# Kernel optimization log

Measured on AMD Instinct MI355X. Metric: run time of the kernel, lower is better.

The kernel has to match this reference:

```python
import jax, jax.numpy as jnp
import numpy as np

EMBED = 1024
HEADS = 16
DIM_HEAD = EMBED // HEADS
N, L = 4, 2048


def setup_inputs() -> dict:
    key = jax.random.key(0)
    ks = jax.random.split(key, 12)
    s = 0.02
    return {
        "q": jax.random.normal(ks[0], (N, L, EMBED), jnp.float32),
        "k": jax.random.normal(ks[1], (N, L, EMBED), jnp.float32),
        "v": jax.random.normal(ks[2], (N, L, EMBED), jnp.float32),
        "padding_mask": jnp.ones((N, L), dtype=bool),
        "sequence_mask": jnp.zeros((L, L), dtype=bool),
        # Linear(in, out): store weight as [out, in] like torch, bias [out]
        "Wq": jax.random.normal(ks[3], (EMBED, EMBED), jnp.float32) * s,
        "bq": jnp.zeros((EMBED,), jnp.float32),
        "Wk": jax.random.normal(ks[4], (EMBED, EMBED), jnp.float32) * s,
        "bk": jnp.zeros((EMBED,), jnp.float32),
        "Wv": jax.random.normal(ks[5], (EMBED, EMBED), jnp.float32) * s,
        "bv": jnp.zeros((EMBED,), jnp.float32),
        "Wo": jax.random.normal(ks[6], (EMBED, EMBED), jnp.float32) * s,
        "bo": jnp.zeros((EMBED,), jnp.float32),
    }


def reference(q, k, v, padding_mask, sequence_mask, Wq, bq, Wk, bk, Wv, bv, Wo, bo):
    n, lq, _ = q.shape
    lk = k.shape[1]
    # input projections
    qp = (q @ Wq.T + bq).reshape(n, lq, HEADS, DIM_HEAD)
    kp = (k @ Wk.T + bk).reshape(n, lk, HEADS, DIM_HEAD)
    vp = (v @ Wv.T + bv).reshape(n, lk, HEADS, DIM_HEAD)
    # energy: [n, h, lq, lk]
    energy = jnp.einsum('nqhd,nkhd->nhqk', qp, kp)
    attention = jax.nn.softmax(energy / jnp.sqrt(jnp.float32(EMBED)), axis=3)
    # NOTE: the original torch code calls masked_fill (non in-place) and
    # discards the result, so padding_mask / sequence_mask have NO effect.
    # Dropout is also never applied in forward. Replicated faithfully.
    out = jnp.einsum('nhqk,nkhd->nqhd', attention, vp)
    out = out.reshape(n, lq, EMBED)
    return out @ Wo.T + bo
```

## Files before the change

kernel.cpp:

```cpp
#include <hip/hip_runtime.h>
#include <stdint.h>

typedef _Float16 f16;
typedef _Float16 f16x8 __attribute__((ext_vector_type(8)));
typedef _Float16 f16x4 __attribute__((ext_vector_type(4)));
typedef _Float16 f16x2 __attribute__((ext_vector_type(2)));
typedef float f32x4 __attribute__((ext_vector_type(4)));

__device__ __forceinline__ f32x4 mfma16(f16x8 a, f16x8 b, f32x4 c) {
    return __builtin_amdgcn_mfma_f32_16x16x32_f16(a, b, c, 0, 0, 0);
}

__device__ __forceinline__ void gload16(const f16* g, f16* l) {
    __builtin_amdgcn_global_load_lds(
        (const __attribute__((address_space(1))) uint32_t*)g,
        (__attribute__((address_space(3))) uint32_t*)l, 16, 0, 0);
}

template <bool OUT16>
__device__ __forceinline__ void gemm_body(const f16* __restrict__ A,
                                          const f16* __restrict__ B,
                                          const float* __restrict__ bias,
                                          void* __restrict__ Cout, long ldo,
                                          int biasrow, float scale,
                                          long m0, long n0, f16* As, f16* Bs) {
    int tid = threadIdx.x;
    int lane = tid & 63, w = tid >> 6;
    int wm = w & 1, wn = w >> 1;
    int l15 = lane & 15, quad = lane >> 4;

    int rg = lane >> 3;
    int cg = (lane & 7) ^ rg;
    const f16* ag[4];
    const f16* bg[4];
    f16* al[4];
    f16* bl[4];
#pragma unroll
    for (int t = 0; t < 4; ++t) {
        int rb = (w * 4 + t) * 8;
        ag[t] = A + (m0 + rb + rg) * 1024 + cg * 8;
        bg[t] = B + (n0 + rb + rg) * 1024 + cg * 8;
        al[t] = &As[rb * 64];
        bl[t] = &Bs[rb * 64];
    }

    f32x4 acc[4][4] = {};

    for (int k0 = 0; k0 < 1024; k0 += 64) {
        __syncthreads();
#pragma unroll
        for (int t = 0; t < 4; ++t) {
            gload16(ag[t] + k0, al[t]);
            gload16(bg[t] + k0, bl[t]);
        }
        __syncthreads();
#pragma unroll
        for (int ks = 0; ks < 2; ++ks) {
            int cc = (ks * 4 + quad) ^ (l15 & 7);
            f16x8 af[4], bf[4];
#pragma unroll
            for (int t = 0; t < 4; ++t) {
                af[t] = *(const f16x8*)&As[(wm * 64 + t * 16 + l15) * 64 + cc * 8];
                bf[t] = *(const f16x8*)&Bs[(wn * 64 + t * 16 + l15) * 64 + cc * 8];
            }
#pragma unroll
            for (int i = 0; i < 4; ++i)
#pragma unroll
                for (int j = 0; j < 4; ++j)
                    acc[i][j] = mfma16(af[i], bf[j], acc[i][j]);
        }
    }

#pragma unroll
    for (int i = 0; i < 4; ++i) {
        int mrow = wm * 64 + i * 16 + quad * 4;
#pragma unroll
        for (int j = 0; j < 4; ++j) {
            int ncol = wn * 64 + j * 16 + l15;
            long gn = n0 + ncol;
#pragma unroll
            for (int r = 0; r < 4; ++r) {
                long gm = m0 + mrow + r;
                float v = (acc[i][j][r] + (biasrow ? bias[gm] : bias[gn])) * scale;
                if constexpr (OUT16)
                    ((f16*)Cout)[gm * ldo + gn] = (f16)v;
                else
                    ((float*)Cout)[gm * ldo + gn] = v;
            }
        }
    }
}

__global__ __launch_bounds__(256, 2) void qkv_proj(
    const f16* __restrict__ qh, const f16* __restrict__ kh,
    const f16* __restrict__ vh, const f16* __restrict__ Wh,
    const float* __restrict__ bq, const float* __restrict__ bk,
    const float* __restrict__ bv, f16* __restrict__ Qp, f16* __restrict__ Kp,
    f16* __restrict__ Vt) {
    __shared__ __align__(16) f16 As[128 * 64];
    __shared__ __align__(16) f16 Bs[128 * 64];
    int z = blockIdx.z;
    const f16* A;
    const f16* B;
    const float* bias;
    f16* C;
    long ldo;
    int biasrow;
    float scale;
    if (z == 0) {
        A = qh; B = Wh; bias = bq; C = Qp; ldo = 1024; biasrow = 0;
        scale = 0.0450842200277786f;
    } else if (z == 1) {
        A = kh; B = Wh + 1048576; bias = bk; C = Kp; ldo = 1024; biasrow = 0;
        scale = 1.0f;
    } else {
        A = Wh + 2097152; B = vh; bias = bv; C = Vt; ldo = 8192; biasrow = 1;
        scale = 1.0f;
    }
    long m0 = (long)(z == 2 ? blockIdx.y : blockIdx.x) * 128;
    long n0 = (long)(z == 2 ? blockIdx.x : blockIdx.y) * 128;
    gemm_body<true>(A, B, bias, C, ldo, biasrow, scale, m0, n0, As, Bs);
}

__global__ __launch_bounds__(256, 2) void o_proj(const f16* __restrict__ Op,
                                                 const f16* __restrict__ Wo,
                                                 const float* __restrict__ bo,
                                                 float* __restrict__ out) {
    __shared__ __align__(16) f16 As[128 * 64];
    __shared__ __align__(16) f16 Bs[128 * 64];
    gemm_body<false>(Op, Wo, bo, out, 1024, 0, 1.0f, (long)blockIdx.x * 128,
                     (long)blockIdx.y * 128, As, Bs);
}

__global__ __launch_bounds__(256, 2) void attn256(const f16* __restrict__ Qp,
                                                  const f16* __restrict__ Kp,
                                                  const f16* __restrict__ Vt,
                                                  f16* __restrict__ Op) {
    __shared__ __align__(16) f16 Ps0[128 * 64];
    __shared__ __align__(16) f16 Ps1[128 * 64];
    __shared__ __align__(16) f16 Ks[2][64 * 64];
    __shared__ __align__(16) f16 Vs[2][64 * 64];

    int tid = threadIdx.x;
    int lane = tid & 63, w = tid >> 6;
    int l15 = lane & 15, quad = lane >> 4;
    int b = blockIdx.x;
    int xcd = b & 7, slot = b >> 3;
    int nh = xcd * 8 + (slot >> 3);
    int qp = slot & 7;
    int nb = nh >> 4, h = nh & 15;
    long tok0 = (long)nb * 2048;
    long qrow0 = qp * 256;

    int rg = lane >> 3, cg = (lane & 7) ^ rg;

    const f16* qsrc0 = Qp + (tok0 + qrow0) * 1024 + h * 64;
    const f16* qsrc1 = qsrc0 + 128 * 1024;
#pragma unroll
    for (int t = 0; t < 4; ++t) {
        int rb = w * 32 + t * 8;
        gload16(qsrc0 + (rb + rg) * 1024 + cg * 8, &Ps0[rb * 64]);
        gload16(qsrc1 + (rb + rg) * 1024 + cg * 8, &Ps1[rb * 64]);
    }
    const f16* kptr = Kp + (tok0 + w * 16 + rg) * 1024 + h * 64 + cg * 8;
    const f16* vptr = Vt + ((long)h * 64 + w * 16 + rg) * 8192 + tok0 + cg * 8;
    gload16(kptr, &Ks[0][(w * 16) * 64]);
    gload16(kptr + 8 * 1024, &Ks[0][(w * 16 + 8) * 64]);
    gload16(vptr, &Vs[0][(w * 16) * 64]);
    gload16(vptr + (long)8 * 8192, &Vs[0][(w * 16 + 8) * 64]);
    const f16* kn = kptr + 65536;
    const f16* vn = vptr + 64;
    __syncthreads();

    f16x8 qf0[2][2], qf1[2][2];
#pragma unroll
    for (int ks = 0; ks < 2; ++ks) {
        int cc = (ks * 4 + quad) ^ (l15 & 7);
#pragma unroll
        for (int j = 0; j < 2; ++j) {
            qf0[ks][j] = *(const f16x8*)&Ps0[(w * 32 + j * 16 + l15) * 64 + cc * 8];
            qf1[ks][j] = *(const f16x8*)&Ps1[(w * 32 + j * 16 + l15) * 64 + cc * 8];
        }
    }

    f32x4 oacc0[2][4] = {}, oacc1[2][4] = {};
    float rs0[2] = {0.f, 0.f}, rs1[2] = {0.f, 0.f};
    const f32x4 z4 = {0.f, 0.f, 0.f, 0.f};

    for (int kt = 0; kt < 32; ++kt) {
        int cur = kt & 1;
        f32x4 sacc0[4][2], sacc1[4][2];
#pragma unroll
        for (int ks = 0; ks < 2; ++ks) {
            int cc = (ks * 4 + quad) ^ (l15 & 7);
            f16x8 a[4];
#pragma unroll
            for (int t = 0; t < 4; ++t)
                a[t] = *(const f16x8*)&Ks[cur][(t * 16 + l15) * 64 + cc * 8];
#pragma unroll
            for (int i = 0; i < 4; ++i)
#pragma unroll
                for (int j = 0; j < 2; ++j) {
                    if (ks == 0) {
                        sacc0[i][j] = mfma16(a[i], qf0[0][j], z4);
                        sacc1[i][j] = mfma16(a[i], qf1[0][j], z4);
                    } else {
                        sacc0[i][j] = mfma16(a[i], qf0[1][j], sacc0[i][j]);
                        sacc1[i][j] = mfma16(a[i], qf1[1][j], sacc1[i][j]);
                    }
                }
        }
        if (kt < 31) {
            int nxt = cur ^ 1;
            f16* kd = &Ks[nxt][(w * 16) * 64];
            f16* vd = &Vs[nxt][(w * 16) * 64];
            gload16(kn, kd);
            gload16(kn + 8 * 1024, kd + 8 * 64);
            gload16(vn, vd);
            gload16(vn + (long)8 * 8192, vd + 8 * 64);
            kn += 65536;
            vn += 64;
        }
#pragma unroll
        for (int i = 0; i < 4; ++i) {
#pragma unroll
            for (int j = 0; j < 2; ++j) {
                int qrow = w * 32 + j * 16 + l15;
                int kl = i * 16 + quad * 4;
                int c = kl >> 3;
                int off = qrow * 64 + ((c ^ (qrow & 7)) << 3) + (kl & 7);
                {
                    float p0 = __builtin_amdgcn_exp2f(sacc0[i][j][0]);
                    float p1 = __builtin_amdgcn_exp2f(sacc0[i][j][1]);
                    float p2 = __builtin_amdgcn_exp2f(sacc0[i][j][2]);
                    float p3 = __builtin_amdgcn_exp2f(sacc0[i][j][3]);
                    rs0[j] += (p0 + p1) + (p2 + p3);
                    f16x2 lo = __builtin_bit_cast(f16x2, __builtin_amdgcn_cvt_pkrtz(p0, p1));
                    f16x2 hi = __builtin_bit_cast(f16x2, __builtin_amdgcn_cvt_pkrtz(p2, p3));
                    f16x4 ph;
                    ph[0] = lo[0]; ph[1] = lo[1]; ph[2] = hi[0]; ph[3] = hi[1];
                    *(f16x4*)&Ps0[off] = ph;
                }
                {
                    float p0 = __builtin_amdgcn_exp2f(sacc1[i][j][0]);
                    float p1 = __builtin_amdgcn_exp2f(sacc1[i][j][1]);
                    float p2 = __builtin_amdgcn_exp2f(sacc1[i][j][2]);
                    float p3 = __builtin_amdgcn_exp2f(sacc1[i][j][3]);
                    rs1[j] += (p0 + p1) + (p2 + p3);
                    f16x2 lo = __builtin_bit_cast(f16x2, __builtin_amdgcn_cvt_pkrtz(p0, p1));
                    f16x2 hi = __builtin_bit_cast(f16x2, __builtin_amdgcn_cvt_pkrtz(p2, p3));
                    f16x4 ph;
                    ph[0] = lo[0]; ph[1] = lo[1]; ph[2] = hi[0]; ph[3] = hi[1];
                    *(f16x4*)&Ps1[off] = ph;
                }
            }
        }
#pragma unroll
        for (int ks = 0; ks < 2; ++ks) {
            int cc = (ks * 4 + quad) ^ (l15 & 7);
            f16x8 bf[4];
#pragma unroll
            for (int j = 0; j < 4; ++j)
                bf[j] = *(const f16x8*)&Vs[cur][(j * 16 + l15) * 64 + cc * 8];
            f16x8 af0[2], af1[2];
#pragma unroll
            for (int i = 0; i < 2; ++i) {
                af0[i] = *(const f16x8*)&Ps0[(w * 32 + i * 16 + l15) * 64 + cc * 8];
                af1[i] = *(const f16x8*)&Ps1[(w * 32 + i * 16 + l15) * 64 + cc * 8];
            }
#pragma unroll
            for (int i = 0; i < 2; ++i)
#pragma unroll
                for (int j = 0; j < 4; ++j) {
                    oacc0[i][j] = mfma16(af0[i], bf[j], oacc0[i][j]);
                    oacc1[i][j] = mfma16(af1[i], bf[j], oacc1[i][j]);
                }
        }
        __syncthreads();
    }

    float* lsi = (float*)&Ks[0][0];
#pragma unroll
    for (int j = 0; j < 2; ++j) {
        rs0[j] += __shfl_xor(rs0[j], 16, 64);
        rs0[j] += __shfl_xor(rs0[j], 32, 64);
        rs1[j] += __shfl_xor(rs1[j], 16, 64);
        rs1[j] += __shfl_xor(rs1[j], 32, 64);
    }
    if (lane < 16) {
        lsi[w * 32 + lane] = 1.0f / rs0[0];
        lsi[w * 32 + 16 + lane] = 1.0f / rs0[1];
        lsi[128 + w * 32 + lane] = 1.0f / rs1[0];
        lsi[128 + w * 32 + 16 + lane] = 1.0f / rs1[1];
    }

    long otok = tok0 + qrow0;
#pragma unroll
    for (int i = 0; i < 2; ++i) {
        int qrow = w * 32 + i * 16 + quad * 4;
#pragma unroll
        for (int j = 0; j < 4; ++j) {
            int d = j * 16 + l15;
#pragma unroll
            for (int r = 0; r < 4; ++r) {
                Op[(otok + qrow + r) * 1024 + h * 64 + d] =
                    (f16)(oacc0[i][j][r] * lsi[qrow + r]);
                Op[(otok + 128 + qrow + r) * 1024 + h * 64 + d] =
                    (f16)(oacc1[i][j][r] * lsi[128 + qrow + r]);
            }
        }
    }
}

__global__ void cvt_all(const float* __restrict__ q, const float* __restrict__ k,
                        const float* __restrict__ v, const float* __restrict__ w0,
                        const float* __restrict__ w1, const float* __restrict__ w2,
                        const float* __restrict__ w3, f16* __restrict__ qh,
                        f16* __restrict__ kh, f16* __restrict__ vh,
                        f16* __restrict__ wh) {
    long id = (long)blockIdx.x * 256 + threadIdx.x;
    const float* s;
    f16* d;
    long off;
    if (id < 3145728) {
        int which = (int)(id >> 20);
        off = (id & 1048575) * 8;
        s = which == 0 ? q : which == 1 ? k : v;
        d = which == 0 ? qh : which == 1 ? kh : vh;
    } else {
        long id2 = id - 3145728;
        int wi = (int)(id2 >> 17);
        off = (id2 & 131071) * 8;
        s = wi == 0 ? w0 : wi == 1 ? w1 : wi == 2 ? w2 : w3;
        d = wh + (long)wi * 1048576;
    }
    f32x4 a = *(const f32x4*)(s + off);
    f32x4 b = *(const f32x4*)(s + off + 4);
    f16x8 hv;
    hv[0] = (f16)a[0]; hv[1] = (f16)a[1]; hv[2] = (f16)a[2]; hv[3] = (f16)a[3];
    hv[4] = (f16)b[0]; hv[5] = (f16)b[1]; hv[6] = (f16)b[2]; hv[7] = (f16)b[3];
    *(f16x8*)(d + off) = hv;
}

extern "C" void kernel_launch(void* const* d_in, const int* in_sizes, int n_in,
                              void* d_out, int out_size, void* d_ws, size_t ws_size,
                              hipStream_t stream) {
    const float* q  = (const float*)d_in[0];
    const float* k  = (const float*)d_in[1];
    const float* v  = (const float*)d_in[2];
    const float* Wq = (const float*)d_in[5];
    const float* bq = (const float*)d_in[6];
    const float* Wk = (const float*)d_in[7];
    const float* bk = (const float*)d_in[8];
    const float* Wv = (const float*)d_in[9];
    const float* bv = (const float*)d_in[10];
    const float* Wo = (const float*)d_in[11];
    const float* bo = (const float*)d_in[12];

    char* ws = (char*)d_ws;
    f16* qh = (f16*)ws;
    f16* kh = (f16*)(ws + (16L << 20));
    f16* vh = (f16*)(ws + (32L << 20));
    f16* Wh = (f16*)(ws + (48L << 20));
    f16* Qp = (f16*)(ws + (56L << 20));
    f16* Kp = (f16*)(ws + (72L << 20));
    f16* Vt = (f16*)(ws + (88L << 20));
    f16* Op = (f16*)(ws + (104L << 20));

    cvt_all<<<14336, 256, 0, stream>>>(q, k, v, Wq, Wk, Wv, Wo, qh, kh, vh, Wh);

    qkv_proj<<<dim3(64, 8, 3), 256, 0, stream>>>(qh, kh, vh, Wh, bq, bk, bv,
                                                 Qp, Kp, Vt);

    attn256<<<512, 256, 0, stream>>>(Qp, Kp, Vt, Op);

    o_proj<<<dim3(64, 8), 256, 0, stream>>>(Op, Wh + 3145728, bo, (float*)d_out);
}
```

Before: 340.2 us.

## Share one P buffer across two query halves to fit three attention blocks per CU

Attention now uses a single P tile in LDS instead of two. The second query half is staged through the unused K/V double-buffer slots at startup, and its exp/PV phase is serialized after the first half's. This cuts LDS per block so launch bounds can request three blocks per CU instead of two. It also adds s_setprio around the MFMA sections to favour matrix work across waves. The cost is more serialization inside each iteration and higher register pressure under the tighter occupancy bound.

```diff
diff --git a/kernel.cpp b/kernel.cpp
--- a/kernel.cpp
+++ b/kernel.cpp
@@ -132,12 +132,11 @@
                      (long)blockIdx.y * 128, As, Bs);
 }
 
-__global__ __launch_bounds__(256, 2) void attn256(const f16* __restrict__ Qp,
+__global__ __launch_bounds__(256, 3) void attn256(const f16* __restrict__ Qp,
                                                   const f16* __restrict__ Kp,
                                                   const f16* __restrict__ Vt,
                                                   f16* __restrict__ Op) {
-    __shared__ __align__(16) f16 Ps0[128 * 64];
-    __shared__ __align__(16) f16 Ps1[128 * 64];
+    __shared__ __align__(16) f16 Ps[128 * 64];
     __shared__ __align__(16) f16 Ks[2][64 * 64];
     __shared__ __align__(16) f16 Vs[2][64 * 64];
 
@@ -159,8 +158,9 @@
 #pragma unroll
     for (int t = 0; t < 4; ++t) {
         int rb = w * 32 + t * 8;
-        gload16(qsrc0 + (rb + rg) * 1024 + cg * 8, &Ps0[rb * 64]);
-        gload16(qsrc1 + (rb + rg) * 1024 + cg * 8, &Ps1[rb * 64]);
+        gload16(qsrc0 + (rb + rg) * 1024 + cg * 8, &Ps[rb * 64]);
+        f16* q1d = (rb < 64) ? &Ks[1][rb * 64] : &Vs[1][(rb - 64) * 64];
+        gload16(qsrc1 + (rb + rg) * 1024 + cg * 8, q1d);
     }
     const f16* kptr = Kp + (tok0 + w * 16 + rg) * 1024 + h * 64 + cg * 8;
     const f16* vptr = Vt + ((long)h * 64 + w * 16 + rg) * 8192 + tok0 + cg * 8;
@@ -173,15 +173,19 @@
     __syncthreads();
 
     f16x8 qf0[2][2], qf1[2][2];
+    const f16* q1b = (w < 2) ? &Ks[1][0] : &Vs[1][0];
+    int q1off = (w < 2) ? 0 : 64;
 #pragma unroll
     for (int ks = 0; ks < 2; ++ks) {
         int cc = (ks * 4 + quad) ^ (l15 & 7);
 #pragma unroll
         for (int j = 0; j < 2; ++j) {
-            qf0[ks][j] = *(const f16x8*)&Ps0[(w * 32 + j * 16 + l15) * 64 + cc * 8];
-            qf1[ks][j] = *(const f16x8*)&Ps1[(w * 32 + j * 16 + l15) * 64 + cc * 8];
-        }
-    }
+            int row = w * 32 + j * 16 + l15;
+            qf0[ks][j] = *(const f16x8*)&Ps[row * 64 + cc * 8];
+            qf1[ks][j] = *(const f16x8*)&q1b[(row - q1off) * 64 + cc * 8];
+        }
+    }
+    __syncthreads();
 
     f32x4 oacc0[2][4] = {}, oacc1[2][4] = {};
     float rs0[2] = {0.f, 0.f}, rs1[2] = {0.f, 0.f};
@@ -190,6 +194,7 @@
     for (int kt = 0; kt < 32; ++kt) {
         int cur = kt & 1;
         f32x4 sacc0[4][2], sacc1[4][2];
+        __builtin_amdgcn_s_setprio(1);
 #pragma unroll
         for (int ks = 0; ks < 2; ++ks) {
             int cc = (ks * 4 + quad) ^ (l15 & 7);
@@ -210,6 +215,7 @@
                     }
                 }
         }
+        __builtin_amdgcn_s_setprio(0);
         if (kt < 31) {
             int nxt = cur ^ 1;
             f16* kd = &Ks[nxt][(w * 16) * 64];
@@ -229,32 +235,19 @@
                 int kl = i * 16 + quad * 4;
                 int c = kl >> 3;
                 int off = qrow * 64 + ((c ^ (qrow & 7)) << 3) + (kl & 7);
-                {
-                    float p0 = __builtin_amdgcn_exp2f(sacc0[i][j][0]);
-                    float p1 = __builtin_amdgcn_exp2f(sacc0[i][j][1]);
-                    float p2 = __builtin_amdgcn_exp2f(sacc0[i][j][2]);
-                    float p3 = __builtin_amdgcn_exp2f(sacc0[i][j][3]);
-                    rs0[j] += (p0 + p1) + (p2 + p3);
-                    f16x2 lo = __builtin_bit_cast(f16x2, __builtin_amdgcn_cvt_pkrtz(p0, p1));
-                    f16x2 hi = __builtin_bit_cast(f16x2, __builtin_amdgcn_cvt_pkrtz(p2, p3));
-                    f16x4 ph;
-                    ph[0] = lo[0]; ph[1] = lo[1]; ph[2] = hi[0]; ph[3] = hi[1];
-                    *(f16x4*)&Ps0[off] = ph;
-                }
-                {
-                    float p0 = __builtin_amdgcn_exp2f(sacc1[i][j][0]);
-                    float p1 = __builtin_amdgcn_exp2f(sacc1[i][j][1]);
-                    float p2 = __builtin_amdgcn_exp2f(sacc1[i][j][2]);
-                    float p3 = __builtin_amdgcn_exp2f(sacc1[i][j][3]);
-                    rs1[j] += (p0 + p1) + (p2 + p3);
-                    f16x2 lo = __builtin_bit_cast(f16x2, __builtin_amdgcn_cvt_pkrtz(p0, p1));
-                    f16x2 hi = __builtin_bit_cast(f16x2, __builtin_amdgcn_cvt_pkrtz(p2, p3));
-                    f16x4 ph;
-                    ph[0] = lo[0]; ph[1] = lo[1]; ph[2] = hi[0]; ph[3] = hi[1];
-                    *(f16x4*)&Ps1[off] = ph;
-                }
+                float p0 = __builtin_amdgcn_exp2f(sacc0[i][j][0]);
+                float p1 = __builtin_amdgcn_exp2f(sacc0[i][j][1]);
+                float p2 = __builtin_amdgcn_exp2f(sacc0[i][j][2]);
+                float p3 = __builtin_amdgcn_exp2f(sacc0[i][j][3]);
+                rs0[j] += (p0 + p1) + (p2 + p3);
+                f16x2 lo = __builtin_bit_cast(f16x2, __builtin_amdgcn_cvt_pkrtz(p0, p1));
+                f16x2 hi = __builtin_bit_cast(f16x2, __builtin_amdgcn_cvt_pkrtz(p2, p3));
+                f16x4 ph;
+                ph[0] = lo[0]; ph[1] = lo[1]; ph[2] = hi[0]; ph[3] = hi[1];
+                *(f16x4*)&Ps[off] = ph;
             }
         }
+        __builtin_amdgcn_s_setprio(1);
 #pragma unroll
         for (int ks = 0; ks < 2; ++ks) {
             int cc = (ks * 4 + quad) ^ (l15 & 7);
@@ -262,20 +255,56 @@
 #pragma unroll
             for (int j = 0; j < 4; ++j)
                 bf[j] = *(const f16x8*)&Vs[cur][(j * 16 + l15) * 64 + cc * 8];
-            f16x8 af0[2], af1[2];
-#pragma unroll
-            for (int i = 0; i < 2; ++i) {
-                af0[i] = *(const f16x8*)&Ps0[(w * 32 + i * 16 + l15) * 64 + cc * 8];
-                af1[i] = *(const f16x8*)&Ps1[(w * 32 + i * 16 + l15) * 64 + cc * 8];
+            f16x8 af0[2];
+#pragma unroll
+            for (int i = 0; i < 2; ++i)
+                af0[i] = *(const f16x8*)&Ps[(w * 32 + i * 16 + l15) * 64 + cc * 8];
+#pragma unroll
+            for (int i = 0; i < 2; ++i)
+#pragma unroll
+                for (int j = 0; j < 4; ++j)
+                    oacc0[i][j] = mfma16(af0[i], bf[j], oacc0[i][j]);
+        }
+        __builtin_amdgcn_s_setprio(0);
+#pragma unroll
+        for (int i = 0; i < 4; ++i) {
+#pragma unroll
+            for (int j = 0; j < 2; ++j) {
+                int qrow = w * 32 + j * 16 + l15;
+                int kl = i * 16 + quad * 4;
+                int c = kl >> 3;
+                int off = qrow * 64 + ((c ^ (qrow & 7)) << 3) + (kl & 7);
+                float p0 = __builtin_amdgcn_exp2f(sacc1[i][j][0]);
+                float p1 = __builtin_amdgcn_exp2f(sacc1[i][j][1]);
+                float p2 = __builtin_amdgcn_exp2f(sacc1[i][j][2]);
+                float p3 = __builtin_amdgcn_exp2f(sacc1[i][j][3]);
+                rs1[j] += (p0 + p1) + (p2 + p3);
+                f16x2 lo = __builtin_bit_cast(f16x2, __builtin_amdgcn_cvt_pkrtz(p0, p1));
+                f16x2 hi = __builtin_bit_cast(f16x2, __builtin_amdgcn_cvt_pkrtz(p2, p3));
+                f16x4 ph;
+                ph[0] = lo[0]; ph[1] = lo[1]; ph[2] = hi[0]; ph[3] = hi[1];
+                *(f16x4*)&Ps[off] = ph;
             }
+        }
+        __builtin_amdgcn_s_setprio(1);
+#pragma unroll
+        for (int ks = 0; ks < 2; ++ks) {
+            int cc = (ks * 4 + quad) ^ (l15 & 7);
+            f16x8 bf[4];
+#pragma unroll
+            for (int j = 0; j < 4; ++j)
+                bf[j] = *(const f16x8*)&Vs[cur][(j * 16 + l15) * 64 + cc * 8];
+            f16x8 af1[2];
 #pragma unroll
             for (int i = 0; i < 2; ++i)
-#pragma unroll
-                for (int j = 0; j < 4; ++j) {
-                    oacc0[i][j] = mfma16(af0[i], bf[j], oacc0[i][j]);
+                af1[i] = *(const f16x8*)&Ps[(w * 32 + i * 16 + l15) * 64 + cc * 8];
+#pragma unroll
+            for (int i = 0; i < 2; ++i)
+#pragma unroll
+                for (int j = 0; j < 4; ++j)
                     oacc1[i][j] = mfma16(af1[i], bf[j], oacc1[i][j]);
-                }
-        }
+        }
+        __builtin_amdgcn_s_setprio(0);
         __syncthreads();
     }
 
```

Result: slower. 475.7 us (+39.8%).

## Halve attention query tile to 128 rows and add MFMA priority hints

Applied to the files above, without the earlier changes.

The attention kernel now processes 128 query rows per block instead of 256 and launches twice as many blocks. This cuts register and LDS use per block and gives more parallelism across the GPU's CUs. In exchange, each K/V tile is reused by fewer queries, so K/V traffic from L2/HBM doubles. It also wraps the MFMA sections in s_setprio so matrix work is prioritised over the exp/softmax phase of other waves.

```diff
diff --git a/kernel.cpp b/kernel.cpp
--- a/kernel.cpp
+++ b/kernel.cpp
@@ -132,12 +132,11 @@
                      (long)blockIdx.y * 128, As, Bs);
 }
 
-__global__ __launch_bounds__(256, 2) void attn256(const f16* __restrict__ Qp,
+__global__ __launch_bounds__(256, 2) void attn128(const f16* __restrict__ Qp,
                                                   const f16* __restrict__ Kp,
                                                   const f16* __restrict__ Vt,
                                                   f16* __restrict__ Op) {
-    __shared__ __align__(16) f16 Ps0[128 * 64];
-    __shared__ __align__(16) f16 Ps1[128 * 64];
+    __shared__ __align__(16) f16 Ps[128 * 64];
     __shared__ __align__(16) f16 Ks[2][64 * 64];
     __shared__ __align__(16) f16 Vs[2][64 * 64];
 
@@ -146,21 +145,19 @@
     int l15 = lane & 15, quad = lane >> 4;
     int b = blockIdx.x;
     int xcd = b & 7, slot = b >> 3;
-    int nh = xcd * 8 + (slot >> 3);
-    int qp = slot & 7;
+    int nh = xcd * 8 + (slot >> 4);
+    int qt = slot & 15;
     int nb = nh >> 4, h = nh & 15;
     long tok0 = (long)nb * 2048;
-    long qrow0 = qp * 256;
+    long qrow0 = (long)qt * 128;
 
     int rg = lane >> 3, cg = (lane & 7) ^ rg;
 
-    const f16* qsrc0 = Qp + (tok0 + qrow0) * 1024 + h * 64;
-    const f16* qsrc1 = qsrc0 + 128 * 1024;
+    const f16* qsrc = Qp + (tok0 + qrow0) * 1024 + h * 64;
 #pragma unroll
     for (int t = 0; t < 4; ++t) {
         int rb = w * 32 + t * 8;
-        gload16(qsrc0 + (rb + rg) * 1024 + cg * 8, &Ps0[rb * 64]);
-        gload16(qsrc1 + (rb + rg) * 1024 + cg * 8, &Ps1[rb * 64]);
+        gload16(qsrc + (rb + rg) * 1024 + cg * 8, &Ps[rb * 64]);
     }
     const f16* kptr = Kp + (tok0 + w * 16 + rg) * 1024 + h * 64 + cg * 8;
     const f16* vptr = Vt + ((long)h * 64 + w * 16 + rg) * 8192 + tok0 + cg * 8;
@@ -172,24 +169,23 @@
     const f16* vn = vptr + 64;
     __syncthreads();
 
-    f16x8 qf0[2][2], qf1[2][2];
+    f16x8 qf[2][2];
 #pragma unroll
     for (int ks = 0; ks < 2; ++ks) {
         int cc = (ks * 4 + quad) ^ (l15 & 7);
 #pragma unroll
-        for (int j = 0; j < 2; ++j) {
-            qf0[ks][j] = *(const f16x8*)&Ps0[(w * 32 + j * 16 + l15) * 64 + cc * 8];
-            qf1[ks][j] = *(const f16x8*)&Ps1[(w * 32 + j * 16 + l15) * 64 + cc * 8];
-        }
-    }
-
-    f32x4 oacc0[2][4] = {}, oacc1[2][4] = {};
-    float rs0[2] = {0.f, 0.f}, rs1[2] = {0.f, 0.f};
+        for (int j = 0; j < 2; ++j)
+            qf[ks][j] = *(const f16x8*)&Ps[(w * 32 + j * 16 + l15) * 64 + cc * 8];
+    }
+
+    f32x4 oacc[2][4] = {};
+    float rs[2] = {0.f, 0.f};
     const f32x4 z4 = {0.f, 0.f, 0.f, 0.f};
 
     for (int kt = 0; kt < 32; ++kt) {
         int cur = kt & 1;
-        f32x4 sacc0[4][2], sacc1[4][2];
+        f32x4 sacc[4][2];
+        __builtin_amdgcn_s_setprio(1);
 #pragma unroll
         for (int ks = 0; ks < 2; ++ks) {
             int cc = (ks * 4 + quad) ^ (l15 & 7);
@@ -201,23 +197,19 @@
             for (int i = 0; i < 4; ++i)
 #pragma unroll
                 for (int j = 0; j < 2; ++j) {
-                    if (ks == 0) {
-                        sacc0[i][j] = mfma16(a[i], qf0[0][j], z4);
-                        sacc1[i][j] = mfma16(a[i], qf1[0][j], z4);
-                    } else {
-                        sacc0[i][j] = mfma16(a[i], qf0[1][j], sacc0[i][j]);
-                        sacc1[i][j] = mfma16(a[i], qf1[1][j], sacc1[i][j]);
-                    }
+                    if (ks == 0)
+                        sacc[i][j] = mfma16(a[i], qf[0][j], z4);
+                    else
+                        sacc[i][j] = mfma16(a[i], qf[1][j], sacc[i][j]);
                 }
         }
+        __builtin_amdgcn_s_setprio(0);
         if (kt < 31) {
             int nxt = cur ^ 1;
-            f16* kd = &Ks[nxt][(w * 16) * 64];
-            f16* vd = &Vs[nxt][(w * 16) * 64];
-            gload16(kn, kd);
-            gload16(kn + 8 * 1024, kd + 8 * 64);
-            gload16(vn, vd);
-            gload16(vn + (long)8 * 8192, vd + 8 * 64);
+            gload16(kn, &Ks[nxt][(w * 16) * 64]);
+            gload16(kn + 8 * 1024, &Ks[nxt][(w * 16 + 8) * 64]);
+            gload16(vn, &Vs[nxt][(w * 16) * 64]);
+            gload16(vn + (long)8 * 8192, &Vs[nxt][(w * 16 + 8) * 64]);
             kn += 65536;
             vn += 64;
         }
@@ -229,32 +221,19 @@
                 int kl = i * 16 + quad * 4;
                 int c = kl >> 3;
                 int off = qrow * 64 + ((c ^ (qrow & 7)) << 3) + (kl & 7);
-                {
-                    float p0 = __builtin_amdgcn_exp2f(sacc0[i][j][0]);
-                    float p1 = __builtin_amdgcn_exp2f(sacc0[i][j][1]);
-                    float p2 = __builtin_amdgcn_exp2f(sacc0[i][j][2]);
-                    float p3 = __builtin_amdgcn_exp2f(sacc0[i][j][3]);
-                    rs0[j] += (p0 + p1) + (p2 + p3);
-                    f16x2 lo = __builtin_bit_cast(f16x2, __builtin_amdgcn_cvt_pkrtz(p0, p1));
-                    f16x2 hi = __builtin_bit_cast(f16x2, __builtin_amdgcn_cvt_pkrtz(p2, p3));
-                    f16x4 ph;
-                    ph[0] = lo[0]; ph[1] = lo[1]; ph[2] = hi[0]; ph[3] = hi[1];
-                    *(f16x4*)&Ps0[off] = ph;
-                }
-                {
-                    float p0 = __builtin_amdgcn_exp2f(sacc1[i][j][0]);
-                    float p1 = __builtin_amdgcn_exp2f(sacc1[i][j][1]);
-                    float p2 = __builtin_amdgcn_exp2f(sacc1[i][j][2]);
-                    float p3 = __builtin_amdgcn_exp2f(sacc1[i][j][3]);
-                    rs1[j] += (p0 + p1) + (p2 + p3);
-                    f16x2 lo = __builtin_bit_cast(f16x2, __builtin_amdgcn_cvt_pkrtz(p0, p1));
-                    f16x2 hi = __builtin_bit_cast(f16x2, __builtin_amdgcn_cvt_pkrtz(p2, p3));
-                    f16x4 ph;
-                    ph[0] = lo[0]; ph[1] = lo[1]; ph[2] = hi[0]; ph[3] = hi[1];
-                    *(f16x4*)&Ps1[off] = ph;
-                }
+                float p0 = __builtin_amdgcn_exp2f(sacc[i][j][0]);
+                float p1 = __builtin_amdgcn_exp2f(sacc[i][j][1]);
+                float p2 = __builtin_amdgcn_exp2f(sacc[i][j][2]);
+                float p3 = __builtin_amdgcn_exp2f(sacc[i][j][3]);
+                rs[j] += (p0 + p1) + (p2 + p3);
+                f16x2 lo = __builtin_bit_cast(f16x2, __builtin_amdgcn_cvt_pkrtz(p0, p1));
+                f16x2 hi = __builtin_bit_cast(f16x2, __builtin_amdgcn_cvt_pkrtz(p2, p3));
+                f16x4 ph;
+                ph[0] = lo[0]; ph[1] = lo[1]; ph[2] = hi[0]; ph[3] = hi[1];
+                *(f16x4*)&Ps[off] = ph;
             }
         }
+        __builtin_amdgcn_s_setprio(1);
 #pragma unroll
         for (int ks = 0; ks < 2; ++ks) {
             int cc = (ks * 4 + quad) ^ (l15 & 7);
@@ -262,36 +241,29 @@
 #pragma unroll
             for (int j = 0; j < 4; ++j)
                 bf[j] = *(const f16x8*)&Vs[cur][(j * 16 + l15) * 64 + cc * 8];
-            f16x8 af0[2], af1[2];
-#pragma unroll
-            for (int i = 0; i < 2; ++i) {
-                af0[i] = *(const f16x8*)&Ps0[(w * 32 + i * 16 + l15) * 64 + cc * 8];
-                af1[i] = *(const f16x8*)&Ps1[(w * 32 + i * 16 + l15) * 64 + cc * 8];
-            }
+            f16x8 af[2];
 #pragma unroll
             for (int i = 0; i < 2; ++i)
-#pragma unroll
-                for (int j = 0; j < 4; ++j) {
-                    oacc0[i][j] = mfma16(af0[i], bf[j], oacc0[i][j]);
-                    oacc1[i][j] = mfma16(af1[i], bf[j], oacc1[i][j]);
-                }
-        }
+                af[i] = *(const f16x8*)&Ps[(w * 32 + i * 16 + l15) * 64 + cc * 8];
+#pragma unroll
+            for (int i = 0; i < 2; ++i)
+#pragma unroll
+                for (int j = 0; j < 4; ++j)
+                    oacc[i][j] = mfma16(af[i], bf[j], oacc[i][j]);
+        }
+        __builtin_amdgcn_s_setprio(0);
         __syncthreads();
     }
 
     float* lsi = (float*)&Ks[0][0];
 #pragma unroll
     for (int j = 0; j < 2; ++j) {
-        rs0[j] += __shfl_xor(rs0[j], 16, 64);
-        rs0[j] += __shfl_xor(rs0[j], 32, 64);
-        rs1[j] += __shfl_xor(rs1[j], 16, 64);
-        rs1[j] += __shfl_xor(rs1[j], 32, 64);
+        rs[j] += __shfl_xor(rs[j], 16, 64);
+        rs[j] += __shfl_xor(rs[j], 32, 64);
     }
     if (lane < 16) {
-        lsi[w * 32 + lane] = 1.0f / rs0[0];
-        lsi[w * 32 + 16 + lane] = 1.0f / rs0[1];
-        lsi[128 + w * 32 + lane] = 1.0f / rs1[0];
-        lsi[128 + w * 32 + 16 + lane] = 1.0f / rs1[1];
+        lsi[w * 32 + lane] = 1.0f / rs[0];
+        lsi[w * 32 + 16 + lane] = 1.0f / rs[1];
     }
 
     long otok = tok0 + qrow0;
@@ -304,9 +276,7 @@
 #pragma unroll
             for (int r = 0; r < 4; ++r) {
                 Op[(otok + qrow + r) * 1024 + h * 64 + d] =
-                    (f16)(oacc0[i][j][r] * lsi[qrow + r]);
-                Op[(otok + 128 + qrow + r) * 1024 + h * 64 + d] =
-                    (f16)(oacc1[i][j][r] * lsi[128 + qrow + r]);
+                    (f16)(oacc[i][j][r] * lsi[qrow + r]);
             }
         }
     }
@@ -372,7 +342,7 @@
     qkv_proj<<<dim3(64, 8, 3), 256, 0, stream>>>(qh, kh, vh, Wh, bq, bk, bv,
                                                  Qp, Kp, Vt);
 
-    attn256<<<512, 256, 0, stream>>>(Qp, Kp, Vt, Op);
+    attn128<<<1024, 256, 0, stream>>>(Qp, Kp, Vt, Op);
 
     o_proj<<<dim3(64, 8), 256, 0, stream>>>(Op, Wh + 3145728, bo, (float*)d_out);
 }
```

New measurement: 349.7 us. 1.03x slower.

## Load K/V and Q fragments directly from global, drop LDS staging and block barriers

Applied to the files above, without the earlier changes.

The attention kernel stops staging K and V tiles in double-buffered LDS via global_load_lds and removes the per-iteration __syncthreads. Each wave now reads its K, V and Q MFMA fragments straight from global memory (relying on L2/L1 reuse across waves), keeping LDS only for the per-wave P tiles. It also wraps the MFMA phases in s_setprio raises and makes the row-sum scratch per-wave. This removes barrier stalls and LDS traffic, but each of the four waves now fetches the same K/V data separately with strided 16-byte global loads, and those loads are no longer prefetched ahead of use.

```diff
diff --git a/kernel.cpp b/kernel.cpp
--- a/kernel.cpp
+++ b/kernel.cpp
@@ -138,8 +138,6 @@
                                                   f16* __restrict__ Op) {
     __shared__ __align__(16) f16 Ps0[128 * 64];
     __shared__ __align__(16) f16 Ps1[128 * 64];
-    __shared__ __align__(16) f16 Ks[2][64 * 64];
-    __shared__ __align__(16) f16 Vs[2][64 * 64];
 
     int tid = threadIdx.x;
     int lane = tid & 63, w = tid >> 6;
@@ -152,51 +150,33 @@
     long tok0 = (long)nb * 2048;
     long qrow0 = qp * 256;
 
-    int rg = lane >> 3, cg = (lane & 7) ^ rg;
-
-    const f16* qsrc0 = Qp + (tok0 + qrow0) * 1024 + h * 64;
-    const f16* qsrc1 = qsrc0 + 128 * 1024;
-#pragma unroll
-    for (int t = 0; t < 4; ++t) {
-        int rb = w * 32 + t * 8;
-        gload16(qsrc0 + (rb + rg) * 1024 + cg * 8, &Ps0[rb * 64]);
-        gload16(qsrc1 + (rb + rg) * 1024 + cg * 8, &Ps1[rb * 64]);
-    }
-    const f16* kptr = Kp + (tok0 + w * 16 + rg) * 1024 + h * 64 + cg * 8;
-    const f16* vptr = Vt + ((long)h * 64 + w * 16 + rg) * 8192 + tok0 + cg * 8;
-    gload16(kptr, &Ks[0][(w * 16) * 64]);
-    gload16(kptr + 8 * 1024, &Ks[0][(w * 16 + 8) * 64]);
-    gload16(vptr, &Vs[0][(w * 16) * 64]);
-    gload16(vptr + (long)8 * 8192, &Vs[0][(w * 16 + 8) * 64]);
-    const f16* kn = kptr + 65536;
-    const f16* vn = vptr + 64;
-    __syncthreads();
-
+    const f16* qbase = Qp + (tok0 + qrow0) * 1024 + h * 64;
     f16x8 qf0[2][2], qf1[2][2];
 #pragma unroll
-    for (int ks = 0; ks < 2; ++ks) {
-        int cc = (ks * 4 + quad) ^ (l15 & 7);
+    for (int ks = 0; ks < 2; ++ks)
 #pragma unroll
         for (int j = 0; j < 2; ++j) {
-            qf0[ks][j] = *(const f16x8*)&Ps0[(w * 32 + j * 16 + l15) * 64 + cc * 8];
-            qf1[ks][j] = *(const f16x8*)&Ps1[(w * 32 + j * 16 + l15) * 64 + cc * 8];
-        }
-    }
+            long row = w * 32 + j * 16 + l15;
+            qf0[ks][j] = *(const f16x8*)&qbase[row * 1024 + ks * 32 + quad * 8];
+            qf1[ks][j] = *(const f16x8*)&qbase[(row + 128) * 1024 + ks * 32 + quad * 8];
+        }
 
     f32x4 oacc0[2][4] = {}, oacc1[2][4] = {};
     float rs0[2] = {0.f, 0.f}, rs1[2] = {0.f, 0.f};
     const f32x4 z4 = {0.f, 0.f, 0.f, 0.f};
 
+    const f16* kkt = Kp + tok0 * 1024 + h * 64;
+    const f16* vkt = Vt + ((long)h * 64) * 8192 + tok0;
+
     for (int kt = 0; kt < 32; ++kt) {
-        int cur = kt & 1;
         f32x4 sacc0[4][2], sacc1[4][2];
+        __builtin_amdgcn_s_setprio(1);
 #pragma unroll
         for (int ks = 0; ks < 2; ++ks) {
-            int cc = (ks * 4 + quad) ^ (l15 & 7);
             f16x8 a[4];
 #pragma unroll
             for (int t = 0; t < 4; ++t)
-                a[t] = *(const f16x8*)&Ks[cur][(t * 16 + l15) * 64 + cc * 8];
+                a[t] = *(const f16x8*)&kkt[(long)(t * 16 + l15) * 1024 + ks * 32 + quad * 8];
 #pragma unroll
             for (int i = 0; i < 4; ++i)
 #pragma unroll
@@ -210,17 +190,15 @@
                     }
                 }
         }
-        if (kt < 31) {
-            int nxt = cur ^ 1;
-            f16* kd = &Ks[nxt][(w * 16) * 64];
-            f16* vd = &Vs[nxt][(w * 16) * 64];
-            gload16(kn, kd);
-            gload16(kn + 8 * 1024, kd + 8 * 64);
-            gload16(vn, vd);
-            gload16(vn + (long)8 * 8192, vd + 8 * 64);
-            kn += 65536;
-            vn += 64;
-        }
+        __builtin_amdgcn_s_setprio(0);
+
+        f16x8 bf[2][4];
+#pragma unroll
+        for (int ks = 0; ks < 2; ++ks)
+#pragma unroll
+            for (int j = 0; j < 4; ++j)
+                bf[ks][j] = *(const f16x8*)&vkt[(long)(j * 16 + l15) * 8192 + ks * 32 + quad * 8];
+
 #pragma unroll
         for (int i = 0; i < 4; ++i) {
 #pragma unroll
@@ -255,13 +233,11 @@
                 }
             }
         }
+
+        __builtin_amdgcn_s_setprio(1);
 #pragma unroll
         for (int ks = 0; ks < 2; ++ks) {
             int cc = (ks * 4 + quad) ^ (l15 & 7);
-            f16x8 bf[4];
-#pragma unroll
-            for (int j = 0; j < 4; ++j)
-                bf[j] = *(const f16x8*)&Vs[cur][(j * 16 + l15) * 64 + cc * 8];
             f16x8 af0[2], af1[2];
 #pragma unroll
             for (int i = 0; i < 2; ++i) {
@@ -272,14 +248,17 @@
             for (int i = 0; i < 2; ++i)
 #pragma unroll
                 for (int j = 0; j < 4; ++j) {
-                    oacc0[i][j] = mfma16(af0[i], bf[j], oacc0[i][j]);
-                    oacc1[i][j] = mfma16(af1[i], bf[j], oacc1[i][j]);
+                    oacc0[i][j] = mfma16(af0[i], bf[ks][j], oacc0[i][j]);
+                    oacc1[i][j] = mfma16(af1[i], bf[ks][j], oacc1[i][j]);
                 }
         }
-        __syncthreads();
-    }
-
-    float* lsi = (float*)&Ks[0][0];
+        __builtin_amdgcn_s_setprio(0);
+
+        kkt += 64 * 1024;
+        vkt += 64;
+    }
+
+    float* lw = (float*)&Ps0[(w * 32) * 64];
 #pragma unroll
     for (int j = 0; j < 2; ++j) {
         rs0[j] += __shfl_xor(rs0[j], 16, 64);
@@ -288,25 +267,26 @@
         rs1[j] += __shfl_xor(rs1[j], 32, 64);
     }
     if (lane < 16) {
-        lsi[w * 32 + lane] = 1.0f / rs0[0];
-        lsi[w * 32 + 16 + lane] = 1.0f / rs0[1];
-        lsi[128 + w * 32 + lane] = 1.0f / rs1[0];
-        lsi[128 + w * 32 + 16 + lane] = 1.0f / rs1[1];
+        lw[lane] = 1.0f / rs0[0];
+        lw[16 + lane] = 1.0f / rs0[1];
+        lw[32 + lane] = 1.0f / rs1[0];
+        lw[48 + lane] = 1.0f / rs1[1];
     }
 
     long otok = tok0 + qrow0;
 #pragma unroll
     for (int i = 0; i < 2; ++i) {
-        int qrow = w * 32 + i * 16 + quad * 4;
+        int lrow = i * 16 + quad * 4;
+        int qrow = w * 32 + lrow;
 #pragma unroll
         for (int j = 0; j < 4; ++j) {
             int d = j * 16 + l15;
 #pragma unroll
             for (int r = 0; r < 4; ++r) {
                 Op[(otok + qrow + r) * 1024 + h * 64 + d] =
-                    (f16)(oacc0[i][j][r] * lsi[qrow + r]);
+                    (f16)(oacc0[i][j][r] * lw[lrow + r]);
                 Op[(otok + 128 + qrow + r) * 1024 + h * 64 + d] =
-                    (f16)(oacc1[i][j][r] * lsi[128 + qrow + r]);
+                    (f16)(oacc1[i][j][r] * lw[32 + lrow + r]);
             }
         }
     }
```

Result: slower. 388.1 us (+14.1%).
